# Kernel tuning notes

Measured on AMD Instinct MI355X. Metric: run time of the kernel, lower is better.

## Reference

```python
import jax, jax.numpy as jnp
import numpy as np

HEADS = 4
DIM_HEAD = 32


def setup_inputs() -> dict:
    key = jax.random.key(0)
    k0, k1, k2, k3 = jax.random.split(key, 4)
    b, C, H, W = 32, 128, 64, 64
    hidden = HEADS * DIM_HEAD
    x = jax.random.normal(k0, (b, C, H, W), dtype=jnp.float32)
    g = jnp.ones((C,), dtype=jnp.float32)                      # RMSNorm gain
    w_qkv = jax.random.normal(k1, (3 * hidden, C), dtype=jnp.float32) * 0.05
    mem_kv = jax.random.normal(k2, (2, HEADS, DIM_HEAD, 4), dtype=jnp.float32)
    w_out = jax.random.normal(k3, (C, hidden), dtype=jnp.float32) * 0.05
    b_out = jnp.zeros((C,), dtype=jnp.float32)
    return {"x": x, "g": g, "w_qkv": w_qkv, "mem_kv": mem_kv,
            "w_out": w_out, "b_out": b_out}


def reference(x, g, w_qkv, mem_kv, w_out, b_out):
    b, C, H, W = x.shape
    heads = mem_kv.shape[1]
    dh = mem_kv.shape[2]
    hidden = heads * dh
    scale = dh ** -0.5

    # RMSNorm variant: F.normalize along channel dim * g * sqrt(C)
    norm = jnp.maximum(jnp.sqrt(jnp.sum(x * x, axis=1, keepdims=True)), 1e-12)
    xn = x / norm * g[None, :, None, None] * (C ** 0.5)

    # 1x1 conv qkv projection (no bias)
    qkv = jnp.einsum('bchw,oc->bohw', xn, w_qkv)  # [b, 3*hidden, H, W]
    q, k, v = jnp.split(qkv, 3, axis=1)
    n = H * W
    q = q.reshape(b, heads, dh, n)
    k = k.reshape(b, heads, dh, n)
    v = v.reshape(b, heads, dh, n)

    # prepend memory kv slots along the token dim
    mk = jnp.broadcast_to(mem_kv[0][None], (b, heads, dh, mem_kv.shape[3]))
    mv = jnp.broadcast_to(mem_kv[1][None], (b, heads, dh, mem_kv.shape[3]))
    k = jnp.concatenate([mk, k], axis=-1)
    v = jnp.concatenate([mv, v], axis=-1)

    q = jax.nn.softmax(q, axis=-2) * scale   # softmax over feature dim d
    k = jax.nn.softmax(k, axis=-1)           # softmax over token dim n

    context = jnp.einsum('bhdn,bhen->bhde', k, v)   # [b,h,d,e]
    out = jnp.einsum('bhde,bhdn->bhen', context, q)  # [b,h,e,n]
    out = out.reshape(b, hidden, H, W)

    # 1x1 conv output projection (with bias)
    return jnp.einsum('bchw,oc->bohw', out, w_out) + b_out[None, :, None, None]
```

## Files before the change

kernel.cpp:

```cpp
#include <hip/hip_runtime.h>
#include <hip/hip_bf16.h>

typedef __attribute__((ext_vector_type(8))) short short8;
typedef __attribute__((ext_vector_type(4))) short bf16x4;
typedef __attribute__((ext_vector_type(4))) float f32x4;


__device__ __forceinline__ unsigned short f2bf(float f) {
  unsigned u = __float_as_uint(f);
  u += 0x7fff + ((u >> 16) & 1);
  return (unsigned short)(u >> 16);
}
__device__ __forceinline__ float bf2f(unsigned short s) {
  return __uint_as_float(((unsigned)s) << 16);
}

__global__ void k0_init(const float* __restrict__ wqkv, const float* __restrict__ g,
                        float* __restrict__ ws) {
  int tid = blockIdx.x * blockDim.x + threadIdx.x;
  int stride = gridDim.x * blockDim.x;
  unsigned short* Wf = (unsigned short*)(ws + 2424832);
  for (int i = tid; i < 49152; i += stride) {
    int o = i >> 7, c = i & 127;
    int f = (o >> 4) * 4 + (c >> 5);
    int lane = (o & 15) + (((c >> 3) & 3) << 4);
    Wf[f * 512 + lane * 8 + (c & 7)] = f2bf(wqkv[o * 128 + c]);
  }
  float* gs = ws + 2449408;
  if (tid < 128) gs[tid] = g[tid] * 11.313708498984761f;
}

__global__ __launch_bounds__(256, 2) void k1_qkv(
    const float* __restrict__ x, const unsigned short* __restrict__ Wf,
    const float* __restrict__ gs, unsigned short* __restrict__ Sp,
    unsigned short* __restrict__ Zp, unsigned short* __restrict__ qbf) {
  __shared__ __align__(16) unsigned short xnf[16 * 512];
  __shared__ __align__(16) unsigned short kbuf[128 * 64];
  __shared__ __align__(16) unsigned short vbuf[128 * 64];
  __shared__ float ssred[256];
  const int b = blockIdx.x >> 4, grp = blockIdx.x & 15;
  const int tid = threadIdx.x;
  const int p = tid & 63, w = tid >> 6;
  const int chunk = __builtin_amdgcn_readfirstlane(w);
  const int l = p, quad = l >> 4, l16 = l & 15;

  short8 ones;
#pragma unroll
  for (int j = 0; j < 8; j++) ones[j] = (short)0x3F80;

  f32x4 accS[2][2] = {};
  f32x4 accZ[2] = {};

  const float* xbase = x + (size_t)b * 524288;
  float xr[32];
  {
    const float* xb = xbase + grp * 256 + p;
#pragma unroll
    for (int i = 0; i < 32; i++) xr[i] = xb[(size_t)(chunk * 32 + i) * 4096];
  }

#pragma unroll 1
  for (int t = 0; t < 4; t++) {
    const int tile = grp * 4 + t;
    float ss = 0.f;
#pragma unroll
    for (int i = 0; i < 32; i++) ss += xr[i] * xr[i];
    ssred[w * 64 + p] = ss;
    __syncthreads();
    float tot = ssred[p] + ssred[64 + p] + ssred[128 + p] + ssred[192 + p];
    float inv = 1.0f / fmaxf(sqrtf(tot), 1e-12f);
#pragma unroll
    for (int q8 = 0; q8 < 4; q8++) {
      short8 v8;
#pragma unroll
      for (int j = 0; j < 8; j++) {
        int i = q8 * 8 + j;
        v8[j] = (short)f2bf(xr[i] * gs[chunk * 32 + i] * inv);
      }
      *(short8*)&xnf[(chunk * 4 + (p >> 4)) * 512 + ((p & 15) + q8 * 16) * 8] = v8;
    }
    __syncthreads();

    if (t < 3) {
      const float* xb = xbase + (tile + 1) * 64 + p;
#pragma unroll
      for (int i = 0; i < 32; i++) xr[i] = xb[(size_t)(chunk * 32 + i) * 4096];
    }

    const short8* Wfv = (const short8*)Wf;
#pragma unroll
    for (int s = 0; s < 3; s++) {
      f32x4 acc[2][4] = {};
#pragma unroll
      for (int k0 = 0; k0 < 4; k0++) {
        short8 bfr[4];
#pragma unroll
        for (int n0 = 0; n0 < 4; n0++)
          bfr[n0] = *(const short8*)&xnf[(k0 * 4 + n0) * 512 + l * 8];
#pragma unroll
        for (int off = 0; off < 2; off++) {
          short8 afr = Wfv[((s * 8 + chunk * 2 + off) * 4 + k0) * 64 + l];
#pragma unroll
          for (int n0 = 0; n0 < 4; n0++)
            acc[off][n0] = __builtin_amdgcn_mfma_f32_16x16x32_bf16(afr, bfr[n0], acc[off][n0], 0, 0, 0);
        }
      }
      if (s == 0) {
#pragma unroll
        for (int n0 = 0; n0 < 4; n0++) {
          float m = -1e30f;
#pragma unroll
          for (int off = 0; off < 2; off++)
#pragma unroll
            for (int r = 0; r < 4; r++) m = fmaxf(m, acc[off][n0][r]);
          m = fmaxf(m, __shfl_xor(m, 16, 64));
          m = fmaxf(m, __shfl_xor(m, 32, 64));
          float e[2][4]; float sum = 0.f;
#pragma unroll
          for (int off = 0; off < 2; off++)
#pragma unroll
            for (int r = 0; r < 4; r++) {
              e[off][r] = __expf(acc[off][n0][r] - m);
              sum += e[off][r];
            }
          sum += __shfl_xor(sum, 16, 64);
          sum += __shfl_xor(sum, 32, 64);
          float rs = 0.17677669529663687f / sum;
          int qbase = ((b * 64 + tile) * 16 + chunk * 4 + n0) * 512;
#pragma unroll
          for (int off = 0; off < 2; off++) {
            int lane2 = l16 + ((off * 2 + (quad >> 1)) << 4);
            bf16x4 qv;
#pragma unroll
            for (int r = 0; r < 4; r++) qv[r] = (short)f2bf(e[off][r] * rs);
            *(bf16x4*)&qbf[qbase + lane2 * 8 + (quad & 1) * 4] = qv;
          }
        }
      } else if (s == 1) {
#pragma unroll
        for (int off = 0; off < 2; off++)
#pragma unroll
          for (int n0 = 0; n0 < 4; n0++)
#pragma unroll
            for (int r = 0; r < 4; r++) {
              int row = off * 16 + quad * 4 + r;
              int px = n0 * 16 + l16;
              kbuf[(chunk * 32 + row) * 64 + (px ^ ((row & 7) << 3))] = f2bf(__expf(acc[off][n0][r]));
            }
      } else {
#pragma unroll
        for (int off = 0; off < 2; off++)
#pragma unroll
          for (int n0 = 0; n0 < 4; n0++)
#pragma unroll
            for (int r = 0; r < 4; r++) {
              int row = off * 16 + quad * 4 + r;
              int px = n0 * 16 + l16;
              vbuf[(chunk * 32 + row) * 64 + (px ^ ((row & 7) << 3))] = f2bf(acc[off][n0][r]);
            }
      }
    }

    const unsigned short* kb = kbuf + chunk * 2048;
    const unsigned short* vb = vbuf + chunk * 2048;
#pragma unroll
    for (int kk = 0; kk < 2; kk++) {
      int cofs = (kk * 32 + quad * 8) ^ ((l16 & 7) << 3);
      short8 ak[2], av[2];
#pragma unroll
      for (int mm = 0; mm < 2; mm++) {
        ak[mm] = *(const short8*)&kb[(mm * 16 + l16) * 64 + cofs];
        av[mm] = *(const short8*)&vb[(mm * 16 + l16) * 64 + cofs];
      }
#pragma unroll
      for (int mm = 0; mm < 2; mm++) {
#pragma unroll
        for (int nn = 0; nn < 2; nn++)
          accS[mm][nn] = __builtin_amdgcn_mfma_f32_16x16x32_bf16(ak[mm], av[nn], accS[mm][nn], 0, 0, 0);
        accZ[mm] = __builtin_amdgcn_mfma_f32_16x16x32_bf16(ak[mm], ones, accZ[mm], 0, 0, 0);
      }
    }
  }

  unsigned short* Spb = Sp + (size_t)(b * 16 + grp) * 4096 + chunk * 1024;
#pragma unroll
  for (int mm = 0; mm < 2; mm++)
#pragma unroll
    for (int nn = 0; nn < 2; nn++) {
      bf16x4 sv;
#pragma unroll
      for (int r = 0; r < 4; r++) sv[r] = (short)f2bf(accS[mm][nn][r]);
      *(bf16x4*)&Spb[(mm * 2 + nn) * 256 + l * 4] = sv;
    }
  if (l16 == 0) {
#pragma unroll
    for (int mm = 0; mm < 2; mm++) {
      bf16x4 zv;
#pragma unroll
      for (int r = 0; r < 4; r++) zv[r] = (short)f2bf(accZ[mm][r]);
      *(bf16x4*)&Zp[(b * 16 + grp) * 128 + chunk * 32 + mm * 16 + quad * 4] = zv;
    }
  }
}

__global__ void k2_ctx(const unsigned short* __restrict__ Sp, const unsigned short* __restrict__ Zp,
                       const float* __restrict__ memkv, const float* __restrict__ wout,
                       unsigned short* __restrict__ Mtf) {
  __shared__ float C[1024];
  __shared__ float zinv[128];
  const int b = blockIdx.x >> 2, qr = blockIdx.x & 3, tid = threadIdx.x;
  if (tid < 128) {
    float z = 0.f;
#pragma unroll
    for (int g = 0; g < 16; g++) z += bf2f(Zp[(b * 16 + g) * 128 + tid]);
    float zm = 0.f;
#pragma unroll
    for (int j = 0; j < 4; j++) zm += __expf(memkv[tid * 4 + j]);
    zinv[tid] = 1.0f / (z + zm);
  }
  __syncthreads();
  for (int i = tid; i < 1024; i += 256) {
    int idx = qr * 1024 + i;
    int hd = idx >> 5, e = idx & 31, h = hd >> 5, d = hd & 31;
    int fofs = h * 1024 + ((d >> 4) * 2 + (e >> 4)) * 256 + ((e & 15) + ((d >> 2) & 3) * 16) * 4 + (d & 3);
    float s = 0.f;
#pragma unroll
    for (int g = 0; g < 16; g++) s += bf2f(Sp[(size_t)(b * 16 + g) * 4096 + fofs]);
    float sm = 0.f;
#pragma unroll
    for (int j = 0; j < 4; j++)
      sm += __expf(memkv[hd * 4 + j]) * memkv[512 + (h * 32 + e) * 4 + j];
    C[i] = (s + sm) * zinv[hd];
  }
  __syncthreads();
  for (int i = tid; i < 4096; i += 256) {
    int hd = qr * 32 + (i >> 7);
    int o = i & 127, h = hd >> 5;
    float a = 0.f;
#pragma unroll
    for (int e = 0; e < 32; e++) a += wout[o * 128 + h * 32 + e] * C[(i >> 7) * 32 + e];
    int f = (o >> 4) * 4 + (hd >> 5);
    int lane = (o & 15) + (((hd >> 3) & 3) << 4);
    Mtf[(size_t)b * 16384 + f * 512 + lane * 8 + (hd & 7)] = f2bf(a);
  }
}

__global__ __launch_bounds__(256) void k3_out(
    const unsigned short* __restrict__ qbf, const unsigned short* __restrict__ Mtf,
    const float* __restrict__ bout, float* __restrict__ out) {
  __shared__ __align__(16) unsigned short qf[16 * 512];
  __shared__ __align__(16) float obuf[128 * 68];
  const int b = blockIdx.x >> 6, tile = blockIdx.x & 63;
  const int tid = threadIdx.x;
  const int l = tid & 63, quad = l >> 4, l16 = l & 15;
  const int chunk = __builtin_amdgcn_readfirstlane(tid >> 6);
  const short8* qv = (const short8*)qbf;
  const int base = ((b * 64 + tile) * 16) * 64;
#pragma unroll
  for (int r = 0; r < 4; r++) {
    int cid = tid + 256 * r;
    *(short8*)&qf[cid * 8] = qv[base + cid];
  }
  __syncthreads();
  f32x4 acc[2][4] = {};
  const short8* Mv = (const short8*)Mtf;
#pragma unroll
  for (int k0 = 0; k0 < 4; k0++) {
    short8 bfr[4];
#pragma unroll
    for (int n0 = 0; n0 < 4; n0++)
      bfr[n0] = *(const short8*)&qf[(k0 * 4 + n0) * 512 + l * 8];
#pragma unroll
    for (int mm = 0; mm < 2; mm++) {
      short8 afr = Mv[((size_t)b * 32 + (chunk * 2 + mm) * 4 + k0) * 64 + l];
#pragma unroll
      for (int n0 = 0; n0 < 4; n0++)
        acc[mm][n0] = __builtin_amdgcn_mfma_f32_16x16x32_bf16(afr, bfr[n0], acc[mm][n0], 0, 0, 0);
    }
  }
#pragma unroll
  for (int mm = 0; mm < 2; mm++)
#pragma unroll
    for (int r = 0; r < 4; r++) {
      float bv = bout[chunk * 32 + mm * 16 + quad * 4 + r];
#pragma unroll
      for (int n0 = 0; n0 < 4; n0++) {
        int o = chunk * 32 + mm * 16 + quad * 4 + r;
        obuf[o * 68 + n0 * 16 + l16] = acc[mm][n0][r] + bv;
      }
    }
  __syncthreads();
#pragma unroll
  for (int rr = 0; rr < 8; rr++) {
    int idx = tid + 256 * rr;
    int row = idx >> 4, c4 = idx & 15;
    f32x4 v = *(const f32x4*)&obuf[row * 68 + c4 * 4];
    *(f32x4*)&out[((size_t)b * 128 + row) * 4096 + tile * 64 + c4 * 4] = v;
  }
}

extern "C" void kernel_launch(void* const* d_in, const int* in_sizes, int n_in,
                              void* d_out, int out_size, void* d_ws, size_t ws_size,
                              hipStream_t stream) {
  const float* x     = (const float*)d_in[0];
  const float* g     = (const float*)d_in[1];
  const float* wqkv  = (const float*)d_in[2];
  const float* memkv = (const float*)d_in[3];
  const float* wout  = (const float*)d_in[4];
  const float* bout  = (const float*)d_in[5];
  float* out = (float*)d_out;
  float* ws = (float*)d_ws;
  unsigned short* Sp  = (unsigned short*)ws;
  unsigned short* Zp  = (unsigned short*)(ws + 2097152);
  unsigned short* Mtf = (unsigned short*)(ws + 2162688);
  unsigned short* Wf  = (unsigned short*)(ws + 2424832);
  float* gs  = ws + 2449408;
  unsigned short* qbf = (unsigned short*)(ws + 2449536);

  k0_init<<<128, 256, 0, stream>>>(wqkv, g, ws);
  k1_qkv<<<512, 256, 0, stream>>>(x, Wf, gs, Sp, Zp, qbf);
  k2_ctx<<<128, 256, 0, stream>>>(Sp, Zp, memkv, wout, Mtf);
  k3_out<<<2048, 256, 0, stream>>>(qbf, Mtf, bout, out);
}
```

Before: 192.5 us.

## Halve k1 tiles per block, process K/V in half-tiles, stage w_out in LDS

The QKV kernel now covers 2 pixel tiles per block instead of 4 and launches twice as many blocks. It targets 4 blocks per CU: K/V shared buffers are halved and a new XOR swizzle is used, and K and V are computed and consumed in 32-pixel halves to reduce register pressure. The context kernel reduces over 32 partial sums instead of 16 and caches its slice of w_out in padded shared memory. This trades more partial-sum traffic and reduction work for higher occupancy and parallelism.

```diff
diff --git a/kernel.cpp b/kernel.cpp
--- a/kernel.cpp
+++ b/kernel.cpp
@@ -13,6 +13,9 @@
 }
 __device__ __forceinline__ float bf2f(unsigned short s) {
   return __uint_as_float(((unsigned)s) << 16);
+}
+__device__ __forceinline__ int swz(int row, int px) {
+  return row * 32 + ((((px >> 3) ^ ((row >> 1) & 3)) << 3) | (px & 7));
 }
 
 __global__ void k0_init(const float* __restrict__ wqkv, const float* __restrict__ g,
@@ -30,15 +33,15 @@
   if (tid < 128) gs[tid] = g[tid] * 11.313708498984761f;
 }
 
-__global__ __launch_bounds__(256, 2) void k1_qkv(
+__global__ __launch_bounds__(256, 4) void k1_qkv(
     const float* __restrict__ x, const unsigned short* __restrict__ Wf,
     const float* __restrict__ gs, unsigned short* __restrict__ Sp,
     unsigned short* __restrict__ Zp, unsigned short* __restrict__ qbf) {
   __shared__ __align__(16) unsigned short xnf[16 * 512];
-  __shared__ __align__(16) unsigned short kbuf[128 * 64];
-  __shared__ __align__(16) unsigned short vbuf[128 * 64];
+  __shared__ __align__(16) unsigned short kbuf[128 * 32];
+  __shared__ __align__(16) unsigned short vbuf[128 * 32];
   __shared__ float ssred[256];
-  const int b = blockIdx.x >> 4, grp = blockIdx.x & 15;
+  const int b = blockIdx.x >> 5, grp = blockIdx.x & 31;
   const int tid = threadIdx.x;
   const int p = tid & 63, w = tid >> 6;
   const int chunk = __builtin_amdgcn_readfirstlane(w);
@@ -54,14 +57,14 @@
   const float* xbase = x + (size_t)b * 524288;
   float xr[32];
   {
-    const float* xb = xbase + grp * 256 + p;
+    const float* xb = xbase + grp * 128 + p;
 #pragma unroll
     for (int i = 0; i < 32; i++) xr[i] = xb[(size_t)(chunk * 32 + i) * 4096];
   }
 
 #pragma unroll 1
-  for (int t = 0; t < 4; t++) {
-    const int tile = grp * 4 + t;
+  for (int t = 0; t < 2; t++) {
+    const int tile = grp * 2 + t;
     float ss = 0.f;
 #pragma unroll
     for (int i = 0; i < 32; i++) ss += xr[i] * xr[i];
@@ -81,15 +84,14 @@
     }
     __syncthreads();
 
-    if (t < 3) {
+    if (t == 0) {
       const float* xb = xbase + (tile + 1) * 64 + p;
 #pragma unroll
       for (int i = 0; i < 32; i++) xr[i] = xb[(size_t)(chunk * 32 + i) * 4096];
     }
 
     const short8* Wfv = (const short8*)Wf;
-#pragma unroll
-    for (int s = 0; s < 3; s++) {
+    {
       f32x4 acc[2][4] = {};
 #pragma unroll
       for (int k0 = 0; k0 < 4; k0++) {
@@ -99,90 +101,109 @@
           bfr[n0] = *(const short8*)&xnf[(k0 * 4 + n0) * 512 + l * 8];
 #pragma unroll
         for (int off = 0; off < 2; off++) {
-          short8 afr = Wfv[((s * 8 + chunk * 2 + off) * 4 + k0) * 64 + l];
+          short8 afr = Wfv[((chunk * 2 + off) * 4 + k0) * 64 + l];
 #pragma unroll
           for (int n0 = 0; n0 < 4; n0++)
             acc[off][n0] = __builtin_amdgcn_mfma_f32_16x16x32_bf16(afr, bfr[n0], acc[off][n0], 0, 0, 0);
         }
       }
-      if (s == 0) {
-#pragma unroll
-        for (int n0 = 0; n0 < 4; n0++) {
-          float m = -1e30f;
-#pragma unroll
-          for (int off = 0; off < 2; off++)
-#pragma unroll
-            for (int r = 0; r < 4; r++) m = fmaxf(m, acc[off][n0][r]);
-          m = fmaxf(m, __shfl_xor(m, 16, 64));
-          m = fmaxf(m, __shfl_xor(m, 32, 64));
-          float e[2][4]; float sum = 0.f;
-#pragma unroll
-          for (int off = 0; off < 2; off++)
-#pragma unroll
-            for (int r = 0; r < 4; r++) {
-              e[off][r] = __expf(acc[off][n0][r] - m);
-              sum += e[off][r];
-            }
-          sum += __shfl_xor(sum, 16, 64);
-          sum += __shfl_xor(sum, 32, 64);
-          float rs = 0.17677669529663687f / sum;
-          int qbase = ((b * 64 + tile) * 16 + chunk * 4 + n0) * 512;
+#pragma unroll
+      for (int n0 = 0; n0 < 4; n0++) {
+        float m = -1e30f;
+#pragma unroll
+        for (int off = 0; off < 2; off++)
+#pragma unroll
+          for (int r = 0; r < 4; r++) m = fmaxf(m, acc[off][n0][r]);
+        m = fmaxf(m, __shfl_xor(m, 16, 64));
+        m = fmaxf(m, __shfl_xor(m, 32, 64));
+        float e[2][4]; float sum = 0.f;
+#pragma unroll
+        for (int off = 0; off < 2; off++)
+#pragma unroll
+          for (int r = 0; r < 4; r++) {
+            e[off][r] = __expf(acc[off][n0][r] - m);
+            sum += e[off][r];
+          }
+        sum += __shfl_xor(sum, 16, 64);
+        sum += __shfl_xor(sum, 32, 64);
+        float rs = 0.17677669529663687f / sum;
+        int qbase = ((b * 64 + tile) * 16 + chunk * 4 + n0) * 512;
+#pragma unroll
+        for (int off = 0; off < 2; off++) {
+          int lane2 = l16 + ((off * 2 + (quad >> 1)) << 4);
+          bf16x4 qv;
+#pragma unroll
+          for (int r = 0; r < 4; r++) qv[r] = (short)f2bf(e[off][r] * rs);
+          *(bf16x4*)&qbf[qbase + lane2 * 8 + (quad & 1) * 4] = qv;
+        }
+      }
+    }
+
+#pragma unroll
+    for (int h2 = 0; h2 < 2; h2++) {
+      {
+        f32x4 acck[2][2] = {};
+#pragma unroll
+        for (int k0 = 0; k0 < 4; k0++) {
+          short8 bf0 = *(const short8*)&xnf[(k0 * 4 + (h2 * 2 + 0)) * 512 + l * 8];
+          short8 bf1 = *(const short8*)&xnf[(k0 * 4 + (h2 * 2 + 1)) * 512 + l * 8];
 #pragma unroll
           for (int off = 0; off < 2; off++) {
-            int lane2 = l16 + ((off * 2 + (quad >> 1)) << 4);
-            bf16x4 qv;
-#pragma unroll
-            for (int r = 0; r < 4; r++) qv[r] = (short)f2bf(e[off][r] * rs);
-            *(bf16x4*)&qbf[qbase + lane2 * 8 + (quad & 1) * 4] = qv;
+            short8 afr = Wfv[((8 + chunk * 2 + off) * 4 + k0) * 64 + l];
+            acck[off][0] = __builtin_amdgcn_mfma_f32_16x16x32_bf16(afr, bf0, acck[off][0], 0, 0, 0);
+            acck[off][1] = __builtin_amdgcn_mfma_f32_16x16x32_bf16(afr, bf1, acck[off][1], 0, 0, 0);
           }
         }
-      } else if (s == 1) {
 #pragma unroll
         for (int off = 0; off < 2; off++)
 #pragma unroll
-          for (int n0 = 0; n0 < 4; n0++)
+          for (int n0l = 0; n0l < 2; n0l++)
 #pragma unroll
             for (int r = 0; r < 4; r++) {
-              int row = off * 16 + quad * 4 + r;
-              int px = n0 * 16 + l16;
-              kbuf[(chunk * 32 + row) * 64 + (px ^ ((row & 7) << 3))] = f2bf(__expf(acc[off][n0][r]));
+              int row = chunk * 32 + off * 16 + quad * 4 + r;
+              kbuf[swz(row, n0l * 16 + l16)] = f2bf(__expf(acck[off][n0l][r]));
             }
-      } else {
+      }
+      {
+        f32x4 accv[2][2] = {};
+#pragma unroll
+        for (int k0 = 0; k0 < 4; k0++) {
+          short8 bf0 = *(const short8*)&xnf[(k0 * 4 + (h2 * 2 + 0)) * 512 + l * 8];
+          short8 bf1 = *(const short8*)&xnf[(k0 * 4 + (h2 * 2 + 1)) * 512 + l * 8];
+#pragma unroll
+          for (int off = 0; off < 2; off++) {
+            short8 afr = Wfv[((16 + chunk * 2 + off) * 4 + k0) * 64 + l];
+            accv[off][0] = __builtin_amdgcn_mfma_f32_16x16x32_bf16(afr, bf0, accv[off][0], 0, 0, 0);
+            accv[off][1] = __builtin_amdgcn_mfma_f32_16x16x32_bf16(afr, bf1, accv[off][1], 0, 0, 0);
+          }
+        }
 #pragma unroll
         for (int off = 0; off < 2; off++)
 #pragma unroll
-          for (int n0 = 0; n0 < 4; n0++)
+          for (int n0l = 0; n0l < 2; n0l++)
 #pragma unroll
             for (int r = 0; r < 4; r++) {
-              int row = off * 16 + quad * 4 + r;
-              int px = n0 * 16 + l16;
-              vbuf[(chunk * 32 + row) * 64 + (px ^ ((row & 7) << 3))] = f2bf(acc[off][n0][r]);
+              int row = chunk * 32 + off * 16 + quad * 4 + r;
+              vbuf[swz(row, n0l * 16 + l16)] = f2bf(accv[off][n0l][r]);
             }
       }
-    }
-
-    const unsigned short* kb = kbuf + chunk * 2048;
-    const unsigned short* vb = vbuf + chunk * 2048;
-#pragma unroll
-    for (int kk = 0; kk < 2; kk++) {
-      int cofs = (kk * 32 + quad * 8) ^ ((l16 & 7) << 3);
-      short8 ak[2], av[2];
-#pragma unroll
-      for (int mm = 0; mm < 2; mm++) {
-        ak[mm] = *(const short8*)&kb[(mm * 16 + l16) * 64 + cofs];
-        av[mm] = *(const short8*)&vb[(mm * 16 + l16) * 64 + cofs];
-      }
-#pragma unroll
-      for (int mm = 0; mm < 2; mm++) {
-#pragma unroll
-        for (int nn = 0; nn < 2; nn++)
-          accS[mm][nn] = __builtin_amdgcn_mfma_f32_16x16x32_bf16(ak[mm], av[nn], accS[mm][nn], 0, 0, 0);
-        accZ[mm] = __builtin_amdgcn_mfma_f32_16x16x32_bf16(ak[mm], ones, accZ[mm], 0, 0, 0);
-      }
-    }
-  }
-
-  unsigned short* Spb = Sp + (size_t)(b * 16 + grp) * 4096 + chunk * 1024;
+      {
+        const int rowA = chunk * 32 + l16;
+        short8 ak0 = *(const short8*)&kbuf[swz(rowA, quad * 8)];
+        short8 ak1 = *(const short8*)&kbuf[swz(rowA + 16, quad * 8)];
+        short8 av0 = *(const short8*)&vbuf[swz(rowA, quad * 8)];
+        short8 av1 = *(const short8*)&vbuf[swz(rowA + 16, quad * 8)];
+        accS[0][0] = __builtin_amdgcn_mfma_f32_16x16x32_bf16(ak0, av0, accS[0][0], 0, 0, 0);
+        accS[0][1] = __builtin_amdgcn_mfma_f32_16x16x32_bf16(ak0, av1, accS[0][1], 0, 0, 0);
+        accS[1][0] = __builtin_amdgcn_mfma_f32_16x16x32_bf16(ak1, av0, accS[1][0], 0, 0, 0);
+        accS[1][1] = __builtin_amdgcn_mfma_f32_16x16x32_bf16(ak1, av1, accS[1][1], 0, 0, 0);
+        accZ[0] = __builtin_amdgcn_mfma_f32_16x16x32_bf16(ak0, ones, accZ[0], 0, 0, 0);
+        accZ[1] = __builtin_amdgcn_mfma_f32_16x16x32_bf16(ak1, ones, accZ[1], 0, 0, 0);
+      }
+    }
+  }
+
+  unsigned short* Spb = Sp + (size_t)(b * 32 + grp) * 4096 + chunk * 1024;
 #pragma unroll
   for (int mm = 0; mm < 2; mm++)
 #pragma unroll
@@ -198,7 +219,7 @@
       bf16x4 zv;
 #pragma unroll
       for (int r = 0; r < 4; r++) zv[r] = (short)f2bf(accZ[mm][r]);
-      *(bf16x4*)&Zp[(b * 16 + grp) * 128 + chunk * 32 + mm * 16 + quad * 4] = zv;
+      *(bf16x4*)&Zp[(b * 32 + grp) * 128 + chunk * 32 + mm * 16 + quad * 4] = zv;
     }
   }
 }
@@ -208,11 +229,16 @@
                        unsigned short* __restrict__ Mtf) {
   __shared__ float C[1024];
   __shared__ float zinv[128];
+  __shared__ float wl[128 * 33];
   const int b = blockIdx.x >> 2, qr = blockIdx.x & 3, tid = threadIdx.x;
+  for (int i = tid; i < 4096; i += 256) {
+    int o = i >> 5, e = i & 31;
+    wl[o * 33 + e] = wout[o * 128 + qr * 32 + e];
+  }
   if (tid < 128) {
     float z = 0.f;
 #pragma unroll
-    for (int g = 0; g < 16; g++) z += bf2f(Zp[(b * 16 + g) * 128 + tid]);
+    for (int g = 0; g < 32; g++) z += bf2f(Zp[(b * 32 + g) * 128 + tid]);
     float zm = 0.f;
 #pragma unroll
     for (int j = 0; j < 4; j++) zm += __expf(memkv[tid * 4 + j]);
@@ -225,7 +251,7 @@
     int fofs = h * 1024 + ((d >> 4) * 2 + (e >> 4)) * 256 + ((e & 15) + ((d >> 2) & 3) * 16) * 4 + (d & 3);
     float s = 0.f;
 #pragma unroll
-    for (int g = 0; g < 16; g++) s += bf2f(Sp[(size_t)(b * 16 + g) * 4096 + fofs]);
+    for (int g = 0; g < 32; g++) s += bf2f(Sp[(size_t)(b * 32 + g) * 4096 + fofs]);
     float sm = 0.f;
 #pragma unroll
     for (int j = 0; j < 4; j++)
@@ -235,10 +261,10 @@
   __syncthreads();
   for (int i = tid; i < 4096; i += 256) {
     int hd = qr * 32 + (i >> 7);
-    int o = i & 127, h = hd >> 5;
+    int o = i & 127;
     float a = 0.f;
 #pragma unroll
-    for (int e = 0; e < 32; e++) a += wout[o * 128 + h * 32 + e] * C[(i >> 7) * 32 + e];
+    for (int e = 0; e < 32; e++) a += wl[o * 33 + e] * C[(i >> 7) * 32 + e];
     int f = (o >> 4) * 4 + (hd >> 5);
     int lane = (o & 15) + (((hd >> 3) & 3) << 4);
     Mtf[(size_t)b * 16384 + f * 512 + lane * 8 + (hd & 7)] = f2bf(a);
@@ -318,7 +344,7 @@
   unsigned short* qbf = (unsigned short*)(ws + 2449536);
 
   k0_init<<<128, 256, 0, stream>>>(wqkv, g, ws);
-  k1_qkv<<<512, 256, 0, stream>>>(x, Wf, gs, Sp, Zp, qbf);
+  k1_qkv<<<1024, 256, 0, stream>>>(x, Wf, gs, Sp, Zp, qbf);
   k2_ctx<<<128, 256, 0, stream>>>(Sp, Zp, memkv, wout, Mtf);
   k3_out<<<2048, 256, 0, stream>>>(qbf, Mtf, bout, out);
 }
```

Measured after the change: 337.5 us. 1.75x slower.

## Double k1/k2 grid parallelism and drop LDS staging in output kernel

Applied to the files above, without the earlier changes.

k1 now processes 2 tiles per block instead of 4, doubling the grid to 1024 blocks and the number of partial context sums. k2 is restructured into 512 blocks, each handling 8 head-dims: it caches the w_out slice in padded LDS, reduces Z with warp shuffles and sums 32 partials. k3 hoists the M fragment loads ahead of the q staging and writes outputs straight to global memory instead of transposing through LDS. The goal is better occupancy and latency hiding, at the cost of more partial-sum traffic and less coalesced 64-byte output stores.

```diff
diff --git a/kernel.cpp b/kernel.cpp
--- a/kernel.cpp
+++ b/kernel.cpp
@@ -38,7 +38,7 @@
   __shared__ __align__(16) unsigned short kbuf[128 * 64];
   __shared__ __align__(16) unsigned short vbuf[128 * 64];
   __shared__ float ssred[256];
-  const int b = blockIdx.x >> 4, grp = blockIdx.x & 15;
+  const int b = blockIdx.x >> 5, grp = blockIdx.x & 31;
   const int tid = threadIdx.x;
   const int p = tid & 63, w = tid >> 6;
   const int chunk = __builtin_amdgcn_readfirstlane(w);
@@ -54,14 +54,14 @@
   const float* xbase = x + (size_t)b * 524288;
   float xr[32];
   {
-    const float* xb = xbase + grp * 256 + p;
+    const float* xb = xbase + grp * 128 + p;
 #pragma unroll
     for (int i = 0; i < 32; i++) xr[i] = xb[(size_t)(chunk * 32 + i) * 4096];
   }
 
 #pragma unroll 1
-  for (int t = 0; t < 4; t++) {
-    const int tile = grp * 4 + t;
+  for (int t = 0; t < 2; t++) {
+    const int tile = grp * 2 + t;
     float ss = 0.f;
 #pragma unroll
     for (int i = 0; i < 32; i++) ss += xr[i] * xr[i];
@@ -81,7 +81,7 @@
     }
     __syncthreads();
 
-    if (t < 3) {
+    if (t == 0) {
       const float* xb = xbase + (tile + 1) * 64 + p;
 #pragma unroll
       for (int i = 0; i < 32; i++) xr[i] = xb[(size_t)(chunk * 32 + i) * 4096];
@@ -182,7 +182,7 @@
     }
   }
 
-  unsigned short* Spb = Sp + (size_t)(b * 16 + grp) * 4096 + chunk * 1024;
+  unsigned short* Spb = Sp + (size_t)(b * 32 + grp) * 4096 + chunk * 1024;
 #pragma unroll
   for (int mm = 0; mm < 2; mm++)
 #pragma unroll
@@ -198,48 +198,63 @@
       bf16x4 zv;
 #pragma unroll
       for (int r = 0; r < 4; r++) zv[r] = (short)f2bf(accZ[mm][r]);
-      *(bf16x4*)&Zp[(b * 16 + grp) * 128 + chunk * 32 + mm * 16 + quad * 4] = zv;
-    }
-  }
-}
-
-__global__ void k2_ctx(const unsigned short* __restrict__ Sp, const unsigned short* __restrict__ Zp,
-                       const float* __restrict__ memkv, const float* __restrict__ wout,
-                       unsigned short* __restrict__ Mtf) {
-  __shared__ float C[1024];
-  __shared__ float zinv[128];
-  const int b = blockIdx.x >> 2, qr = blockIdx.x & 3, tid = threadIdx.x;
-  if (tid < 128) {
-    float z = 0.f;
-#pragma unroll
-    for (int g = 0; g < 16; g++) z += bf2f(Zp[(b * 16 + g) * 128 + tid]);
+      *(bf16x4*)&Zp[(b * 32 + grp) * 128 + chunk * 32 + mm * 16 + quad * 4] = zv;
+    }
+  }
+}
+
+__global__ __launch_bounds__(256) void k2_ctx(
+    const unsigned short* __restrict__ Sp, const unsigned short* __restrict__ Zp,
+    const float* __restrict__ memkv, const float* __restrict__ wout,
+    unsigned short* __restrict__ Mtf) {
+  __shared__ float wl[128 * 33];
+  __shared__ float Cs[8 * 32];
+  __shared__ float zsh[8];
+  __shared__ float zinv_s[8];
+  const int b = blockIdx.x >> 4, sl = blockIdx.x & 15, tid = threadIdx.x;
+  const int hd0 = sl * 8, h = hd0 >> 5;
+  for (int i = tid; i < 4096; i += 256) {
+    int o = i >> 5, e = i & 31;
+    wl[o * 33 + e] = wout[o * 128 + h * 32 + e];
+  }
+  {
+    int hdi = tid >> 5, g = tid & 31;
+    float zp = bf2f(Zp[(b * 32 + g) * 128 + hd0 + hdi]);
+#pragma unroll
+    for (int s2 = 1; s2 < 32; s2 <<= 1) zp += __shfl_xor(zp, s2, 32);
+    if (g == 0) zsh[hdi] = zp;
+  }
+  __syncthreads();
+  if (tid < 8) {
+    int hd = hd0 + tid;
     float zm = 0.f;
 #pragma unroll
-    for (int j = 0; j < 4; j++) zm += __expf(memkv[tid * 4 + j]);
-    zinv[tid] = 1.0f / (z + zm);
+    for (int j = 0; j < 4; j++) zm += __expf(memkv[hd * 4 + j]);
+    zinv_s[tid] = 1.0f / (zsh[tid] + zm);
+  }
+  __syncthreads();
+  {
+    int hdi = tid >> 5, e = tid & 31;
+    int hd = hd0 + hdi, d = hd & 31;
+    int fofs = h * 1024 + ((d >> 4) * 2 + (e >> 4)) * 256 + ((e & 15) + ((d >> 2) & 3) * 16) * 4 + (d & 3);
+    const unsigned short* Spb = Sp + (size_t)b * 131072 + fofs;
+    float s = 0.f;
+#pragma unroll
+    for (int g = 0; g < 32; g++) s += bf2f(Spb[g * 4096]);
+    float sm = 0.f;
+#pragma unroll
+    for (int j = 0; j < 4; j++)
+      sm += __expf(memkv[hd * 4 + j]) * memkv[512 + (h * 32 + e) * 4 + j];
+    Cs[hdi * 32 + e] = (s + sm) * zinv_s[hdi];
   }
   __syncthreads();
   for (int i = tid; i < 1024; i += 256) {
-    int idx = qr * 1024 + i;
-    int hd = idx >> 5, e = idx & 31, h = hd >> 5, d = hd & 31;
-    int fofs = h * 1024 + ((d >> 4) * 2 + (e >> 4)) * 256 + ((e & 15) + ((d >> 2) & 3) * 16) * 4 + (d & 3);
-    float s = 0.f;
-#pragma unroll
-    for (int g = 0; g < 16; g++) s += bf2f(Sp[(size_t)(b * 16 + g) * 4096 + fofs]);
-    float sm = 0.f;
-#pragma unroll
-    for (int j = 0; j < 4; j++)
-      sm += __expf(memkv[hd * 4 + j]) * memkv[512 + (h * 32 + e) * 4 + j];
-    C[i] = (s + sm) * zinv[hd];
-  }
-  __syncthreads();
-  for (int i = tid; i < 4096; i += 256) {
-    int hd = qr * 32 + (i >> 7);
-    int o = i & 127, h = hd >> 5;
+    int o = i & 127, hdi = i >> 7;
     float a = 0.f;
 #pragma unroll
-    for (int e = 0; e < 32; e++) a += wout[o * 128 + h * 32 + e] * C[(i >> 7) * 32 + e];
-    int f = (o >> 4) * 4 + (hd >> 5);
+    for (int e = 0; e < 32; e++) a += wl[o * 33 + e] * Cs[hdi * 32 + e];
+    int hd = hd0 + hdi;
+    int f = (o >> 4) * 4 + h;
     int lane = (o & 15) + (((hd >> 3) & 3) << 4);
     Mtf[(size_t)b * 16384 + f * 512 + lane * 8 + (hd & 7)] = f2bf(a);
   }
@@ -249,11 +264,17 @@
     const unsigned short* __restrict__ qbf, const unsigned short* __restrict__ Mtf,
     const float* __restrict__ bout, float* __restrict__ out) {
   __shared__ __align__(16) unsigned short qf[16 * 512];
-  __shared__ __align__(16) float obuf[128 * 68];
   const int b = blockIdx.x >> 6, tile = blockIdx.x & 63;
   const int tid = threadIdx.x;
   const int l = tid & 63, quad = l >> 4, l16 = l & 15;
   const int chunk = __builtin_amdgcn_readfirstlane(tid >> 6);
+  const short8* Mv = (const short8*)Mtf;
+  short8 afr[2][4];
+#pragma unroll
+  for (int mm = 0; mm < 2; mm++)
+#pragma unroll
+    for (int k0 = 0; k0 < 4; k0++)
+      afr[mm][k0] = Mv[((size_t)b * 32 + (chunk * 2 + mm) * 4 + k0) * 64 + l];
   const short8* qv = (const short8*)qbf;
   const int base = ((b * 64 + tile) * 16) * 64;
 #pragma unroll
@@ -263,7 +284,6 @@
   }
   __syncthreads();
   f32x4 acc[2][4] = {};
-  const short8* Mv = (const short8*)Mtf;
 #pragma unroll
   for (int k0 = 0; k0 < 4; k0++) {
     short8 bfr[4];
@@ -271,32 +291,22 @@
     for (int n0 = 0; n0 < 4; n0++)
       bfr[n0] = *(const short8*)&qf[(k0 * 4 + n0) * 512 + l * 8];
 #pragma unroll
-    for (int mm = 0; mm < 2; mm++) {
-      short8 afr = Mv[((size_t)b * 32 + (chunk * 2 + mm) * 4 + k0) * 64 + l];
+    for (int mm = 0; mm < 2; mm++)
 #pragma unroll
       for (int n0 = 0; n0 < 4; n0++)
-        acc[mm][n0] = __builtin_amdgcn_mfma_f32_16x16x32_bf16(afr, bfr[n0], acc[mm][n0], 0, 0, 0);
-    }
-  }
+        acc[mm][n0] = __builtin_amdgcn_mfma_f32_16x16x32_bf16(afr[mm][k0], bfr[n0], acc[mm][n0], 0, 0, 0);
+  }
+  float* ob = out + (size_t)b * 524288 + tile * 64;
 #pragma unroll
   for (int mm = 0; mm < 2; mm++)
 #pragma unroll
     for (int r = 0; r < 4; r++) {
-      float bv = bout[chunk * 32 + mm * 16 + quad * 4 + r];
-#pragma unroll
-      for (int n0 = 0; n0 < 4; n0++) {
-        int o = chunk * 32 + mm * 16 + quad * 4 + r;
-        obuf[o * 68 + n0 * 16 + l16] = acc[mm][n0][r] + bv;
-      }
-    }
-  __syncthreads();
-#pragma unroll
-  for (int rr = 0; rr < 8; rr++) {
-    int idx = tid + 256 * rr;
-    int row = idx >> 4, c4 = idx & 15;
-    f32x4 v = *(const f32x4*)&obuf[row * 68 + c4 * 4];
-    *(f32x4*)&out[((size_t)b * 128 + row) * 4096 + tile * 64 + c4 * 4] = v;
-  }
+      int o = chunk * 32 + mm * 16 + quad * 4 + r;
+      float bv = bout[o];
+#pragma unroll
+      for (int n0 = 0; n0 < 4; n0++)
+        ob[(size_t)o * 4096 + n0 * 16 + l16] = acc[mm][n0][r] + bv;
+    }
 }
 
 extern "C" void kernel_launch(void* const* d_in, const int* in_sizes, int n_in,
@@ -318,7 +328,7 @@
   unsigned short* qbf = (unsigned short*)(ws + 2449536);
 
   k0_init<<<128, 256, 0, stream>>>(wqkv, g, ws);
-  k1_qkv<<<512, 256, 0, stream>>>(x, Wf, gs, Sp, Zp, qbf);
-  k2_ctx<<<128, 256, 0, stream>>>(Sp, Zp, memkv, wout, Mtf);
+  k1_qkv<<<1024, 256, 0, stream>>>(x, Wf, gs, Sp, Zp, qbf);
+  k2_ctx<<<512, 256, 0, stream>>>(Sp, Zp, memkv, wout, Mtf);
   k3_out<<<2048, 256, 0, stream>>>(qbf, Mtf, bout, out);
 }
```

New measurement: 240.5 us. 1.25x slower.
